# Performance work log

Measured on AMD Instinct MI355X. Metric: run time of the kernel, lower is better.

The kernel has to match this reference:

```python
import jax, jax.numpy as jnp
import numpy as np

B, N, D = 1024, 100, 768  # N=100 is hard-coded by th_embedding Linear(100,1)
EPS_LN, EPS = 1e-5, 1e-8


def setup_inputs() -> dict:
    key = jax.random.key(0)
    k0, k1, k2 = jax.random.split(key, 3)
    return {
        "x": jax.random.normal(k0, (B, N, D), dtype=jnp.float32),
        "cluster_center": jax.random.normal(k1, (B, 1, D), dtype=jnp.float32),
        "alpha": jnp.ones((1,), dtype=jnp.float32),
        "ln_gamma": jnp.ones((D,), dtype=jnp.float32),
        "ln_beta": jnp.zeros((D,), dtype=jnp.float32),
        "th_w": jax.random.normal(k2, (1, N), dtype=jnp.float32) * 0.1,
        "th_b": jnp.zeros((1,), dtype=jnp.float32),
    }


def reference(x, cluster_center, alpha, ln_gamma, ln_beta, th_w, th_b):
    # LayerNorm over last dim
    mu = jnp.mean(x, axis=-1, keepdims=True)
    var = jnp.mean((x - mu) ** 2, axis=-1, keepdims=True)
    xn = (x - mu) / jnp.sqrt(var + EPS_LN) * ln_gamma + ln_beta  # [B,N,D]

    # pairwise cosine similarity  [B,N,N]
    num = jnp.einsum("bnd,bmd->bnm", xn, xn)
    nrm = jnp.linalg.norm(xn, axis=-1, keepdims=True)            # [B,N,1]
    den = nrm * jnp.swapaxes(nrm, -2, -1)                        # [B,N,N]
    cos_sim = num / (den + EPS)

    # density + min-max normalize  [B,N]
    density = jnp.sum(cos_sim, axis=-1)
    d_max = jnp.max(density, axis=-1, keepdims=True)
    d_min = jnp.min(density, axis=-1, keepdims=True)
    density = (density - d_min) / (d_max - d_min + EPS)

    # learned threshold: Flatten -> Linear(100,1) -> Sigmoid, scaled by alpha
    th = jax.nn.sigmoid(density @ th_w.T + th_b) * alpha         # [B,1]

    # ReLU gate + normalize
    density = jax.nn.relu(density - th)
    density_th = density / (jnp.sum(density, axis=1, keepdims=True) + EPS)

    # weighted shift of cluster center
    distance_map = xn - cluster_center                           # [B,N,D] (broadcast of repeat)
    shift = distance_map * density_th[:, :, None]
    shift_avg = jnp.mean(shift, axis=1, keepdims=True)           # [B,1,D]
    return cluster_center + shift_avg
```

## Files before the change

### kernel.cpp

```cpp
#include <hip/hip_runtime.h>
#include <math.h>

#define BT     1024
#define NROW   100
#define DDIM   768
#define EPS_LN 1e-5f
#define EPSF   1e-8f

#define LDS_BYTES 157876

__device__ __forceinline__ float bflo(unsigned int p) {
    union { unsigned int u; float f; } c; c.u = p << 16; return c.f;
}
__device__ __forceinline__ float bfhi(unsigned int p) {
    union { unsigned int u; float f; } c; c.u = p & 0xFFFF0000u; return c.f;
}
__device__ __forceinline__ unsigned int cvtpk(float lo, float hi) {
    unsigned int r;
    asm("v_cvt_pk_bf16_f32 %0, %1, %2" : "=v"(r) : "v"(lo), "v"(hi));
    return r;
}
__device__ __forceinline__ float wave_sum(float v) {
#pragma unroll
    for (int m = 32; m >= 1; m >>= 1) v += __shfl_xor(v, m, 64);
    return v;
}

#define DPPADD(v, ctrl) \
    v += __int_as_float(__builtin_amdgcn_update_dpp(0, __float_as_int(v), ctrl, 0xf, 0xf, true))

__device__ __forceinline__ float dpp_half_sum(float v) {
    DPPADD(v, 0x111);
    DPPADD(v, 0x112);
    DPPADD(v, 0x114);
    DPPADD(v, 0x118);
    DPPADD(v, 0x142);
    return v;
}
__device__ __forceinline__ float dpp_half_sum_bcast(float v) {
    v = dpp_half_sum(v);
    return __int_as_float(__builtin_amdgcn_ds_swizzle(__float_as_int(v), 0x03E0));
}

extern "C" __global__ void __launch_bounds__(BT, 4)
ccs_kernel(const float* __restrict__ x,
           const float* __restrict__ cc,
           const float* __restrict__ alpha,
           const float* __restrict__ gamma,
           const float* __restrict__ beta,
           const float* __restrict__ thw,
           const float* __restrict__ thb,
           float* __restrict__ out)
{
    extern __shared__ char lds[];
    unsigned int* u   = (unsigned int*)lds;
    float* S    = (float*)(lds + 153600);
    float* nrm  = (float*)(lds + 156672);
    float* dens = (float*)(lds + 157072);
    float* w2   = (float*)(lds + 157472);
    float* Wsh  = (float*)(lds + 157872);

    const int tid = threadIdx.x;
    const int w   = tid >> 6;
    const int l   = tid & 63;
    const int li  = l & 31;
    const int hw  = (w << 1) | (l >> 5);
    const int b   = blockIdx.x;
    const float* xb = x + (size_t)b * (NROW * DDIM);

    const int base = 4 * li;
    const int pcnt = (hw < 4) ? 4 : 3;

    float xf[24];
    {
        const float* xr = xb + hw * DDIM + base;
#pragma unroll
        for (int k = 0; k < 6; ++k)
            *(float4*)&xf[4 * k] = *(const float4*)(xr + 128 * k);
    }

    float thwa = 0.f, thwb = 0.f, alphav = 0.f, thbv = 0.f;
    if (w == 0) {
        thwa = thw[l];
        if (l < NROW - 64) thwb = thw[64 + l];
        alphav = alpha[0];
        thbv   = thb[0];
    }
    float2 ccv = make_float2(0.f, 0.f);
    if (tid < 384) ccv = *(const float2*)(cc + (size_t)b * DDIM + 2 * tid);

    uint2 gpk[3], bpk[3];
#pragma unroll
    for (int k = 0; k < 3; ++k) {
        const float4 g4 = *(const float4*)(gamma + 256 * k + base);
        const float4 g5 = *(const float4*)(gamma + 256 * k + 128 + base);
        const float4 b4 = *(const float4*)(beta  + 256 * k + base);
        const float4 b5 = *(const float4*)(beta  + 256 * k + 128 + base);
        gpk[k].x = cvtpk(g4.x, g4.y); gpk[k].y = cvtpk(g4.z, g4.w);
        bpk[k].x = cvtpk(b4.x, b4.y); bpk[k].y = cvtpk(b4.z, b4.w);
        (void)g5; (void)b5;
    }
    uint2 gp6[6], bp6[6];
#pragma unroll
    for (int k = 0; k < 6; ++k) {
        const float4 g4 = *(const float4*)(gamma + 128 * k + base);
        const float4 b4 = *(const float4*)(beta  + 128 * k + base);
        gp6[k].x = cvtpk(g4.x, g4.y); gp6[k].y = cvtpk(g4.z, g4.w);
        bp6[k].x = cvtpk(b4.x, b4.y); bp6[k].y = cvtpk(b4.z, b4.w);
    }

#pragma unroll
    for (int r = 0; r < 4; ++r) {
        if (r >= pcnt) break;
        const int row = hw + 32 * r;

        float p0 = 0.f, p1 = 0.f;
#pragma unroll
        for (int m = 0; m < 24; ++m) { p0 += xf[m]; p1 = fmaf(xf[m], xf[m], p1); }

        float xn1[24];
        if (r + 1 < pcnt) {
            const float* xr = xb + (row + 32) * DDIM + base;
#pragma unroll
            for (int k = 0; k < 6; ++k)
                *(float4*)&xn1[4 * k] = *(const float4*)(xr + 128 * k);
        }

        p0 = dpp_half_sum_bcast(p0);
        p1 = dpp_half_sum_bcast(p1);
        const float mu   = p0 * (1.0f / DDIM);
        const float var  = p1 * (1.0f / DDIM) - mu * mu;
        const float A    = rsqrtf(var + EPS_LN);
        const float nmuA = -mu * A;

        float q = 0.f;
#pragma unroll
        for (int k = 0; k < 6; ++k) {
            const float g0 = bflo(gp6[k].x), g1 = bfhi(gp6[k].x);
            const float g2 = bflo(gp6[k].y), g3 = bfhi(gp6[k].y);
            const float b0 = bflo(bp6[k].x), b1 = bfhi(bp6[k].x);
            const float b2 = bflo(bp6[k].y), b3 = bfhi(bp6[k].y);
            float t, v;
            t = fmaf(xf[4*k+0], A, nmuA); v = fmaf(t, g0, b0); xf[4*k+0] = v; q = fmaf(v, v, q);
            t = fmaf(xf[4*k+1], A, nmuA); v = fmaf(t, g1, b1); xf[4*k+1] = v; q = fmaf(v, v, q);
            t = fmaf(xf[4*k+2], A, nmuA); v = fmaf(t, g2, b2); xf[4*k+2] = v; q = fmaf(v, v, q);
            t = fmaf(xf[4*k+3], A, nmuA); v = fmaf(t, g3, b3); xf[4*k+3] = v; q = fmaf(v, v, q);
        }
        q = dpp_half_sum_bcast(q);
        const float qc  = fmaxf(q, 1e-30f);
        const float inv = rsqrtf(qc);
        const float nr  = qc * inv;

        unsigned int* ur = u + row * 384 + 2 * li;
#pragma unroll
        for (int k = 0; k < 6; ++k) {
            uint2 pk;
            pk.x = cvtpk(xf[4 * k + 0] * inv, xf[4 * k + 1] * inv);
            pk.y = cvtpk(xf[4 * k + 2] * inv, xf[4 * k + 3] * inv);
            *(uint2*)&ur[64 * k] = pk;
        }
        if (li == 0) nrm[row] = nr;

        if (r + 1 < pcnt) {
#pragma unroll
            for (int m = 0; m < 24; ++m) xf[m] = xn1[m];
        }
    }
    __syncthreads();

    if (tid < 384) {
        float ax = 0.f, ay = 0.f;
        const unsigned int* up = u + tid;
#pragma unroll 4
        for (int n = 0; n < NROW; ++n) {
            const unsigned int pw = up[n * 384];
            ax += bflo(pw); ay += bfhi(pw);
        }
        *(float2*)&S[2 * tid] = make_float2(ax, ay);
    }
    __syncthreads();

    {
        float Sv[24];
#pragma unroll
        for (int k = 0; k < 3; ++k) {
            *(float4*)&Sv[8 * k]     = *(const float4*)&S[256 * k + 8 * li];
            *(float4*)&Sv[8 * k + 4] = *(const float4*)&S[256 * k + 8 * li + 4];
        }
#pragma unroll
        for (int r = 0; r < 4; ++r) {
            if (r >= pcnt) break;
            const int row = hw + 32 * r;
            const unsigned int* ur = u + row * 384 + 4 * li;
            float d = 0.f;
#pragma unroll
            for (int k = 0; k < 3; ++k) {
                const uint4 pw = *(const uint4*)&ur[128 * k];
                d = fmaf(bflo(pw.x), Sv[8*k+0], d); d = fmaf(bfhi(pw.x), Sv[8*k+1], d);
                d = fmaf(bflo(pw.y), Sv[8*k+2], d); d = fmaf(bfhi(pw.y), Sv[8*k+3], d);
                d = fmaf(bflo(pw.z), Sv[8*k+4], d); d = fmaf(bfhi(pw.z), Sv[8*k+5], d);
                d = fmaf(bflo(pw.w), Sv[8*k+6], d); d = fmaf(bfhi(pw.w), Sv[8*k+7], d);
            }
            d = dpp_half_sum(d);
            if (li == 31) dens[row] = d;
        }
    }
    __syncthreads();

    if (w == 0) {
        const float va = dens[l];
        const bool  hb = (l < NROW - 64);
        const float vb = hb ? dens[64 + l] : 0.f;

        float mxv = hb ? fmaxf(va, vb) : va;
        float mnv = hb ? fminf(va, vb) : va;
#pragma unroll
        for (int m = 32; m >= 1; m >>= 1) {
            mxv = fmaxf(mxv, __shfl_xor(mxv, m, 64));
            mnv = fminf(mnv, __shfl_xor(mnv, m, 64));
        }
        const float rng = 1.0f / (mxv - mnv + EPSF);
        const float ra  = (va - mnv) * rng;
        const float rb  = (vb - mnv) * rng;

        float td = ra * thwa + (hb ? rb * thwb : 0.f);
        td = wave_sum(td);
        const float z  = td + thbv;
        const float th = alphav / (1.0f + expf(-z));

        const float ga  = fmaxf(ra - th, 0.f);
        const float gb_ = hb ? fmaxf(rb - th, 0.f) : 0.f;
        const float sg  = wave_sum(ga + gb_);
        const float wf  = 1.0f / (sg + EPSF);

        w2[l] = ga * wf * nrm[l];
        if (hb) w2[64 + l] = gb_ * wf * nrm[64 + l];
        if (l == 0) Wsh[0] = sg * wf;
    }
    __syncthreads();

    if (tid < 384) {
        float ax = 0.f, ay = 0.f;
        const unsigned int* up = u + tid;
#pragma unroll 4
        for (int n = 0; n < NROW; ++n) {
            const float wv = w2[n];
            const unsigned int pw = up[n * 384];
            ax = fmaf(wv, bflo(pw), ax); ay = fmaf(wv, bfhi(pw), ay);
        }
        const float W = Wsh[0];
        float2 o;
        o.x = ccv.x + (ax - ccv.x * W) * (1.0f / NROW);
        o.y = ccv.y + (ay - ccv.y * W) * (1.0f / NROW);
        *(float2*)(out + (size_t)b * DDIM + 2 * tid) = o;
    }
}

extern "C" void kernel_launch(void* const* d_in, const int* in_sizes, int n_in,
                              void* d_out, int out_size, void* d_ws, size_t ws_size,
                              hipStream_t stream) {
    const float* x     = (const float*)d_in[0];
    const float* cc    = (const float*)d_in[1];
    const float* alpha = (const float*)d_in[2];
    const float* gamma = (const float*)d_in[3];
    const float* beta  = (const float*)d_in[4];
    const float* thw   = (const float*)d_in[5];
    const float* thb   = (const float*)d_in[6];
    float* out = (float*)d_out;

    ccs_kernel<<<1024, BT, LDS_BYTES, stream>>>(x, cc, alpha, gamma, beta, thw, thb, out);
}
```

Baseline: 81.19 us.

## Make kernel persistent over four batches and prefetch next batch rows during tail phases

Launches 256 persistent blocks that each handle four batch items instead of one block per item. While the current item runs its reduction, density and weighted-sum phases, each block prefetches the first two rows of the next item into registers so global loads overlap compute. It also drops an unused gamma/beta packing loop. The cost is higher register pressure and an extra barrier per item, and with only 256 blocks on a 256-CU device each CU holds a single 1024-thread block, so within-block overlap must replace the latency hiding that block-level concurrency used to give.

New measurement: 172.9 us. 2.13x slower.

```diff
diff --git a/kernel.cpp b/kernel.cpp
--- a/kernel.cpp
+++ b/kernel.cpp
@@ -2,6 +2,8 @@
 #include <math.h>
 
 #define BT     1024
+#define GRID   256
+#define NITEMS 4
 #define NROW   100
 #define DDIM   768
 #define EPS_LN 1e-5f
@@ -66,17 +68,19 @@
     const int li  = l & 31;
     const int hw  = (w << 1) | (l >> 5);
     const int b   = blockIdx.x;
-    const float* xb = x + (size_t)b * (NROW * DDIM);
-
     const int base = 4 * li;
-    const int pcnt = (hw < 4) ? 4 : 3;
-
-    float xf[24];
+    const bool has4 = (hw < 4);
+    const int pcnt = has4 ? 4 : 3;
+
+    float pf0[24], pf1[24];
     {
-        const float* xr = xb + hw * DDIM + base;
-#pragma unroll
-        for (int k = 0; k < 6; ++k)
-            *(float4*)&xf[4 * k] = *(const float4*)(xr + 128 * k);
+        const float* xr0 = x + (size_t)b * (NROW * DDIM) + hw * DDIM + base;
+        const float* xr1 = x + (size_t)b * (NROW * DDIM) + (hw + 32) * DDIM + base;
+#pragma unroll
+        for (int k = 0; k < 6; ++k) {
+            *(float4*)&pf0[4 * k] = *(const float4*)(xr0 + 128 * k);
+            *(float4*)&pf1[4 * k] = *(const float4*)(xr1 + 128 * k);
+        }
     }
 
     float thwa = 0.f, thwb = 0.f, alphav = 0.f, thbv = 0.f;
@@ -86,20 +90,7 @@
         alphav = alpha[0];
         thbv   = thb[0];
     }
-    float2 ccv = make_float2(0.f, 0.f);
-    if (tid < 384) ccv = *(const float2*)(cc + (size_t)b * DDIM + 2 * tid);
-
-    uint2 gpk[3], bpk[3];
-#pragma unroll
-    for (int k = 0; k < 3; ++k) {
-        const float4 g4 = *(const float4*)(gamma + 256 * k + base);
-        const float4 g5 = *(const float4*)(gamma + 256 * k + 128 + base);
-        const float4 b4 = *(const float4*)(beta  + 256 * k + base);
-        const float4 b5 = *(const float4*)(beta  + 256 * k + 128 + base);
-        gpk[k].x = cvtpk(g4.x, g4.y); gpk[k].y = cvtpk(g4.z, g4.w);
-        bpk[k].x = cvtpk(b4.x, b4.y); bpk[k].y = cvtpk(b4.z, b4.w);
-        (void)g5; (void)b5;
-    }
+
     uint2 gp6[6], bp6[6];
 #pragma unroll
     for (int k = 0; k < 6; ++k) {
@@ -109,23 +100,10 @@
         bp6[k].x = cvtpk(b4.x, b4.y); bp6[k].y = cvtpk(b4.z, b4.w);
     }
 
-#pragma unroll
-    for (int r = 0; r < 4; ++r) {
-        if (r >= pcnt) break;
-        const int row = hw + 32 * r;
-
+    auto process_row = [&](float (&xf)[24], int row) {
         float p0 = 0.f, p1 = 0.f;
 #pragma unroll
         for (int m = 0; m < 24; ++m) { p0 += xf[m]; p1 = fmaf(xf[m], xf[m], p1); }
-
-        float xn1[24];
-        if (r + 1 < pcnt) {
-            const float* xr = xb + (row + 32) * DDIM + base;
-#pragma unroll
-            for (int k = 0; k < 6; ++k)
-                *(float4*)&xn1[4 * k] = *(const float4*)(xr + 128 * k);
-        }
-
         p0 = dpp_half_sum_bcast(p0);
         p1 = dpp_half_sum_bcast(p1);
         const float mu   = p0 * (1.0f / DDIM);
@@ -160,99 +138,133 @@
             *(uint2*)&ur[64 * k] = pk;
         }
         if (li == 0) nrm[row] = nr;
-
-        if (r + 1 < pcnt) {
-#pragma unroll
-            for (int m = 0; m < 24; ++m) xf[m] = xn1[m];
-        }
-    }
-    __syncthreads();
-
-    if (tid < 384) {
-        float ax = 0.f, ay = 0.f;
-        const unsigned int* up = u + tid;
+    };
+
+    for (int it = 0; it < NITEMS; ++it) {
+        const int bi = b + GRID * it;
+        const float* xb = x + (size_t)bi * (NROW * DDIM);
+
+        float2 ccv = make_float2(0.f, 0.f);
+        if (tid < 384) ccv = *(const float2*)(cc + (size_t)bi * DDIM + 2 * tid);
+
+        float A24[24];
+        {
+            const float* xr = xb + (hw + 64) * DDIM + base;
+#pragma unroll
+            for (int k = 0; k < 6; ++k)
+                *(float4*)&A24[4 * k] = *(const float4*)(xr + 128 * k);
+        }
+        process_row(pf0, hw);
+
+        float B24[24];
+        if (has4) {
+            const float* xr = xb + (hw + 96) * DDIM + base;
+#pragma unroll
+            for (int k = 0; k < 6; ++k)
+                *(float4*)&B24[4 * k] = *(const float4*)(xr + 128 * k);
+        }
+        process_row(pf1, hw + 32);
+        process_row(A24, hw + 64);
+        if (has4) process_row(B24, hw + 96);
+
+        if (it + 1 < NITEMS) {
+            const float* xr0 = x + (size_t)(bi + GRID) * (NROW * DDIM) + hw * DDIM + base;
+            const float* xr1 = x + (size_t)(bi + GRID) * (NROW * DDIM) + (hw + 32) * DDIM + base;
+#pragma unroll
+            for (int k = 0; k < 6; ++k) {
+                *(float4*)&pf0[4 * k] = *(const float4*)(xr0 + 128 * k);
+                *(float4*)&pf1[4 * k] = *(const float4*)(xr1 + 128 * k);
+            }
+        }
+        __syncthreads();
+
+        if (tid < 384) {
+            float ax = 0.f, ay = 0.f;
+            const unsigned int* up = u + tid;
 #pragma unroll 4
-        for (int n = 0; n < NROW; ++n) {
-            const unsigned int pw = up[n * 384];
-            ax += bflo(pw); ay += bfhi(pw);
-        }
-        *(float2*)&S[2 * tid] = make_float2(ax, ay);
-    }
-    __syncthreads();
-
-    {
-        float Sv[24];
-#pragma unroll
-        for (int k = 0; k < 3; ++k) {
-            *(float4*)&Sv[8 * k]     = *(const float4*)&S[256 * k + 8 * li];
-            *(float4*)&Sv[8 * k + 4] = *(const float4*)&S[256 * k + 8 * li + 4];
-        }
-#pragma unroll
-        for (int r = 0; r < 4; ++r) {
-            if (r >= pcnt) break;
-            const int row = hw + 32 * r;
-            const unsigned int* ur = u + row * 384 + 4 * li;
-            float d = 0.f;
+            for (int n = 0; n < NROW; ++n) {
+                const unsigned int pw = up[n * 384];
+                ax += bflo(pw); ay += bfhi(pw);
+            }
+            *(float2*)&S[2 * tid] = make_float2(ax, ay);
+        }
+        __syncthreads();
+
+        {
+            float Sv[24];
 #pragma unroll
             for (int k = 0; k < 3; ++k) {
-                const uint4 pw = *(const uint4*)&ur[128 * k];
-                d = fmaf(bflo(pw.x), Sv[8*k+0], d); d = fmaf(bfhi(pw.x), Sv[8*k+1], d);
-                d = fmaf(bflo(pw.y), Sv[8*k+2], d); d = fmaf(bfhi(pw.y), Sv[8*k+3], d);
-                d = fmaf(bflo(pw.z), Sv[8*k+4], d); d = fmaf(bfhi(pw.z), Sv[8*k+5], d);
-                d = fmaf(bflo(pw.w), Sv[8*k+6], d); d = fmaf(bfhi(pw.w), Sv[8*k+7], d);
-            }
-            d = dpp_half_sum(d);
-            if (li == 31) dens[row] = d;
-        }
-    }
-    __syncthreads();
-
-    if (w == 0) {
-        const float va = dens[l];
-        const bool  hb = (l < NROW - 64);
-        const float vb = hb ? dens[64 + l] : 0.f;
-
-        float mxv = hb ? fmaxf(va, vb) : va;
-        float mnv = hb ? fminf(va, vb) : va;
-#pragma unroll
-        for (int m = 32; m >= 1; m >>= 1) {
-            mxv = fmaxf(mxv, __shfl_xor(mxv, m, 64));
-            mnv = fminf(mnv, __shfl_xor(mnv, m, 64));
-        }
-        const float rng = 1.0f / (mxv - mnv + EPSF);
-        const float ra  = (va - mnv) * rng;
-        const float rb  = (vb - mnv) * rng;
-
-        float td = ra * thwa + (hb ? rb * thwb : 0.f);
-        td = wave_sum(td);
-        const float z  = td + thbv;
-        const float th = alphav / (1.0f + expf(-z));
-
-        const float ga  = fmaxf(ra - th, 0.f);
-        const float gb_ = hb ? fmaxf(rb - th, 0.f) : 0.f;
-        const float sg  = wave_sum(ga + gb_);
-        const float wf  = 1.0f / (sg + EPSF);
-
-        w2[l] = ga * wf * nrm[l];
-        if (hb) w2[64 + l] = gb_ * wf * nrm[64 + l];
-        if (l == 0) Wsh[0] = sg * wf;
-    }
-    __syncthreads();
-
-    if (tid < 384) {
-        float ax = 0.f, ay = 0.f;
-        const unsigned int* up = u + tid;
+                *(float4*)&Sv[8 * k]     = *(const float4*)&S[256 * k + 8 * li];
+                *(float4*)&Sv[8 * k + 4] = *(const float4*)&S[256 * k + 8 * li + 4];
+            }
+#pragma unroll
+            for (int r = 0; r < 4; ++r) {
+                if (r >= pcnt) break;
+                const int row = hw + 32 * r;
+                const unsigned int* ur = u + row * 384 + 4 * li;
+                float d = 0.f;
+#pragma unroll
+                for (int k = 0; k < 3; ++k) {
+                    const uint4 pw = *(const uint4*)&ur[128 * k];
+                    d = fmaf(bflo(pw.x), Sv[8*k+0], d); d = fmaf(bfhi(pw.x), Sv[8*k+1], d);
+                    d = fmaf(bflo(pw.y), Sv[8*k+2], d); d = fmaf(bfhi(pw.y), Sv[8*k+3], d);
+                    d = fmaf(bflo(pw.z), Sv[8*k+4], d); d = fmaf(bfhi(pw.z), Sv[8*k+5], d);
+                    d = fmaf(bflo(pw.w), Sv[8*k+6], d); d = fmaf(bfhi(pw.w), Sv[8*k+7], d);
+                }
+                d = dpp_half_sum(d);
+                if (li == 31) dens[row] = d;
+            }
+        }
+        __syncthreads();
+
+        if (w == 0) {
+            const float va = dens[l];
+            const bool  hb = (l < NROW - 64);
+            const float vb = hb ? dens[64 + l] : 0.f;
+
+            float mxv = hb ? fmaxf(va, vb) : va;
+            float mnv = hb ? fminf(va, vb) : va;
+#pragma unroll
+            for (int m = 32; m >= 1; m >>= 1) {
+                mxv = fmaxf(mxv, __shfl_xor(mxv, m, 64));
+                mnv = fminf(mnv, __shfl_xor(mnv, m, 64));
+            }
+            const float rng = 1.0f / (mxv - mnv + EPSF);
+            const float ra  = (va - mnv) * rng;
+            const float rb  = (vb - mnv) * rng;
+
+            float td = ra * thwa + (hb ? rb * thwb : 0.f);
+            td = wave_sum(td);
+            const float z  = td + thbv;
+            const float th = alphav / (1.0f + expf(-z));
+
+            const float ga  = fmaxf(ra - th, 0.f);
+            const float gb_ = hb ? fmaxf(rb - th, 0.f) : 0.f;
+            const float sg  = wave_sum(ga + gb_);
+            const float wf  = 1.0f / (sg + EPSF);
+
+            w2[l] = ga * wf * nrm[l];
+            if (hb) w2[64 + l] = gb_ * wf * nrm[64 + l];
+            if (l == 0) Wsh[0] = sg * wf;
+        }
+        __syncthreads();
+
+        if (tid < 384) {
+            float ax = 0.f, ay = 0.f;
+            const unsigned int* up = u + tid;
 #pragma unroll 4
-        for (int n = 0; n < NROW; ++n) {
-            const float wv = w2[n];
-            const unsigned int pw = up[n * 384];
-            ax = fmaf(wv, bflo(pw), ax); ay = fmaf(wv, bfhi(pw), ay);
-        }
-        const float W = Wsh[0];
-        float2 o;
-        o.x = ccv.x + (ax - ccv.x * W) * (1.0f / NROW);
-        o.y = ccv.y + (ay - ccv.y * W) * (1.0f / NROW);
-        *(float2*)(out + (size_t)b * DDIM + 2 * tid) = o;
+            for (int n = 0; n < NROW; ++n) {
+                const float wv = w2[n];
+                const unsigned int pw = up[n * 384];
+                ax = fmaf(wv, bflo(pw), ax); ay = fmaf(wv, bfhi(pw), ay);
+            }
+            const float W = Wsh[0];
+            float2 o;
+            o.x = ccv.x + (ax - ccv.x * W) * (1.0f / NROW);
+            o.y = ccv.y + (ay - ccv.y * W) * (1.0f / NROW);
+            *(float2*)(out + (size_t)bi * DDIM + 2 * tid) = o;
+        }
+        __syncthreads();
     }
 }
 
@@ -268,5 +280,5 @@
     const float* thb   = (const float*)d_in[6];
     float* out = (float*)d_out;
 
-    ccs_kernel<<<1024, BT, LDS_BYTES, stream>>>(x, cc, alpha, gamma, beta, thw, thb, out);
-}
+    ccs_kernel<<<GRID, BT, LDS_BYTES, stream>>>(x, cc, alpha, gamma, beta, thw, thb, out);
+}
```

## Make kernel persistent over 4 batches with cross-item prefetch of next x rows

Applied to the files above, without the earlier changes.

The grid shrinks from 1024 blocks to 256 persistent blocks, each looping over 4 batch items. The next item's first x rows are prefetched during the last row of the current item, which hides global load latency across items and avoids relaunching blocks. __syncthreads is replaced by a custom lgkmcnt wait plus s_barrier, and dead gamma/beta packing is removed. The risk is serialization inside each block: with only 256 blocks at one block per CU, the cross-block overlap the 1024-block grid used to provide to hide latency is lost.

Result: slower. 100.0 us (+23.2%).

```diff
diff --git a/kernel.cpp b/kernel.cpp
--- a/kernel.cpp
+++ b/kernel.cpp
@@ -2,12 +2,16 @@
 #include <math.h>
 
 #define BT     1024
+#define GRID   256
+#define NITEMS 4
 #define NROW   100
 #define DDIM   768
 #define EPS_LN 1e-5f
 #define EPSF   1e-8f
 
 #define LDS_BYTES 157876
+
+#define TBAR() asm volatile("s_waitcnt lgkmcnt(0)\n\ts_barrier" ::: "memory")
 
 __device__ __forceinline__ float bflo(unsigned int p) {
     union { unsigned int u; float f; } c; c.u = p << 16; return c.f;
@@ -66,14 +70,12 @@
     const int li  = l & 31;
     const int hw  = (w << 1) | (l >> 5);
     const int b   = blockIdx.x;
-    const float* xb = x + (size_t)b * (NROW * DDIM);
-
     const int base = 4 * li;
     const int pcnt = (hw < 4) ? 4 : 3;
 
     float xf[24];
     {
-        const float* xr = xb + hw * DDIM + base;
+        const float* xr = x + (size_t)b * (NROW * DDIM) + hw * DDIM + base;
 #pragma unroll
         for (int k = 0; k < 6; ++k)
             *(float4*)&xf[4 * k] = *(const float4*)(xr + 128 * k);
@@ -86,20 +88,7 @@
         alphav = alpha[0];
         thbv   = thb[0];
     }
-    float2 ccv = make_float2(0.f, 0.f);
-    if (tid < 384) ccv = *(const float2*)(cc + (size_t)b * DDIM + 2 * tid);
-
-    uint2 gpk[3], bpk[3];
-#pragma unroll
-    for (int k = 0; k < 3; ++k) {
-        const float4 g4 = *(const float4*)(gamma + 256 * k + base);
-        const float4 g5 = *(const float4*)(gamma + 256 * k + 128 + base);
-        const float4 b4 = *(const float4*)(beta  + 256 * k + base);
-        const float4 b5 = *(const float4*)(beta  + 256 * k + 128 + base);
-        gpk[k].x = cvtpk(g4.x, g4.y); gpk[k].y = cvtpk(g4.z, g4.w);
-        bpk[k].x = cvtpk(b4.x, b4.y); bpk[k].y = cvtpk(b4.z, b4.w);
-        (void)g5; (void)b5;
-    }
+
     uint2 gp6[6], bp6[6];
 #pragma unroll
     for (int k = 0; k < 6; ++k) {
@@ -109,150 +98,166 @@
         bp6[k].x = cvtpk(b4.x, b4.y); bp6[k].y = cvtpk(b4.z, b4.w);
     }
 
-#pragma unroll
-    for (int r = 0; r < 4; ++r) {
-        if (r >= pcnt) break;
-        const int row = hw + 32 * r;
-
-        float p0 = 0.f, p1 = 0.f;
-#pragma unroll
-        for (int m = 0; m < 24; ++m) { p0 += xf[m]; p1 = fmaf(xf[m], xf[m], p1); }
-
-        float xn1[24];
-        if (r + 1 < pcnt) {
-            const float* xr = xb + (row + 32) * DDIM + base;
-#pragma unroll
-            for (int k = 0; k < 6; ++k)
-                *(float4*)&xn1[4 * k] = *(const float4*)(xr + 128 * k);
-        }
-
-        p0 = dpp_half_sum_bcast(p0);
-        p1 = dpp_half_sum_bcast(p1);
-        const float mu   = p0 * (1.0f / DDIM);
-        const float var  = p1 * (1.0f / DDIM) - mu * mu;
-        const float A    = rsqrtf(var + EPS_LN);
-        const float nmuA = -mu * A;
-
-        float q = 0.f;
-#pragma unroll
-        for (int k = 0; k < 6; ++k) {
-            const float g0 = bflo(gp6[k].x), g1 = bfhi(gp6[k].x);
-            const float g2 = bflo(gp6[k].y), g3 = bfhi(gp6[k].y);
-            const float b0 = bflo(bp6[k].x), b1 = bfhi(bp6[k].x);
-            const float b2 = bflo(bp6[k].y), b3 = bfhi(bp6[k].y);
-            float t, v;
-            t = fmaf(xf[4*k+0], A, nmuA); v = fmaf(t, g0, b0); xf[4*k+0] = v; q = fmaf(v, v, q);
-            t = fmaf(xf[4*k+1], A, nmuA); v = fmaf(t, g1, b1); xf[4*k+1] = v; q = fmaf(v, v, q);
-            t = fmaf(xf[4*k+2], A, nmuA); v = fmaf(t, g2, b2); xf[4*k+2] = v; q = fmaf(v, v, q);
-            t = fmaf(xf[4*k+3], A, nmuA); v = fmaf(t, g3, b3); xf[4*k+3] = v; q = fmaf(v, v, q);
-        }
-        q = dpp_half_sum_bcast(q);
-        const float qc  = fmaxf(q, 1e-30f);
-        const float inv = rsqrtf(qc);
-        const float nr  = qc * inv;
-
-        unsigned int* ur = u + row * 384 + 2 * li;
-#pragma unroll
-        for (int k = 0; k < 6; ++k) {
-            uint2 pk;
-            pk.x = cvtpk(xf[4 * k + 0] * inv, xf[4 * k + 1] * inv);
-            pk.y = cvtpk(xf[4 * k + 2] * inv, xf[4 * k + 3] * inv);
-            *(uint2*)&ur[64 * k] = pk;
-        }
-        if (li == 0) nrm[row] = nr;
-
-        if (r + 1 < pcnt) {
-#pragma unroll
-            for (int m = 0; m < 24; ++m) xf[m] = xn1[m];
-        }
-    }
-    __syncthreads();
-
-    if (tid < 384) {
-        float ax = 0.f, ay = 0.f;
-        const unsigned int* up = u + tid;
-#pragma unroll 4
-        for (int n = 0; n < NROW; ++n) {
-            const unsigned int pw = up[n * 384];
-            ax += bflo(pw); ay += bfhi(pw);
-        }
-        *(float2*)&S[2 * tid] = make_float2(ax, ay);
-    }
-    __syncthreads();
-
-    {
-        float Sv[24];
-#pragma unroll
-        for (int k = 0; k < 3; ++k) {
-            *(float4*)&Sv[8 * k]     = *(const float4*)&S[256 * k + 8 * li];
-            *(float4*)&Sv[8 * k + 4] = *(const float4*)&S[256 * k + 8 * li + 4];
-        }
+    for (int it = 0; it < NITEMS; ++it) {
+        const int bi = b + GRID * it;
+        const float* xb = x + (size_t)bi * (NROW * DDIM);
+
+        float2 ccv = make_float2(0.f, 0.f);
+        if (tid < 384) ccv = *(const float2*)(cc + (size_t)bi * DDIM + 2 * tid);
+
 #pragma unroll
         for (int r = 0; r < 4; ++r) {
             if (r >= pcnt) break;
             const int row = hw + 32 * r;
-            const unsigned int* ur = u + row * 384 + 4 * li;
-            float d = 0.f;
+
+            float p0 = 0.f, p1 = 0.f;
+#pragma unroll
+            for (int m = 0; m < 24; ++m) { p0 += xf[m]; p1 = fmaf(xf[m], xf[m], p1); }
+
+            const bool nx    = (r + 1 < pcnt);
+            const bool nitem = (!nx) && (it + 1 < NITEMS);
+            float xn1[24];
+            if (nx) {
+                const float* xr = xb + (row + 32) * DDIM + base;
+#pragma unroll
+                for (int k = 0; k < 6; ++k)
+                    *(float4*)&xn1[4 * k] = *(const float4*)(xr + 128 * k);
+            } else if (nitem) {
+                const float* xr = x + (size_t)(bi + GRID) * (NROW * DDIM) + hw * DDIM + base;
+#pragma unroll
+                for (int k = 0; k < 6; ++k)
+                    *(float4*)&xn1[4 * k] = *(const float4*)(xr + 128 * k);
+            }
+
+            p0 = dpp_half_sum_bcast(p0);
+            p1 = dpp_half_sum_bcast(p1);
+            const float mu   = p0 * (1.0f / DDIM);
+            const float var  = p1 * (1.0f / DDIM) - mu * mu;
+            const float A    = rsqrtf(var + EPS_LN);
+            const float nmuA = -mu * A;
+
+            float q = 0.f;
+#pragma unroll
+            for (int k = 0; k < 6; ++k) {
+                const float g0 = bflo(gp6[k].x), g1 = bfhi(gp6[k].x);
+                const float g2 = bflo(gp6[k].y), g3 = bfhi(gp6[k].y);
+                const float b0 = bflo(bp6[k].x), b1 = bfhi(bp6[k].x);
+                const float b2 = bflo(bp6[k].y), b3 = bfhi(bp6[k].y);
+                float t, v;
+                t = fmaf(xf[4*k+0], A, nmuA); v = fmaf(t, g0, b0); xf[4*k+0] = v; q = fmaf(v, v, q);
+                t = fmaf(xf[4*k+1], A, nmuA); v = fmaf(t, g1, b1); xf[4*k+1] = v; q = fmaf(v, v, q);
+                t = fmaf(xf[4*k+2], A, nmuA); v = fmaf(t, g2, b2); xf[4*k+2] = v; q = fmaf(v, v, q);
+                t = fmaf(xf[4*k+3], A, nmuA); v = fmaf(t, g3, b3); xf[4*k+3] = v; q = fmaf(v, v, q);
+            }
+            q = dpp_half_sum_bcast(q);
+            const float qc  = fmaxf(q, 1e-30f);
+            const float inv = rsqrtf(qc);
+            const float nr  = qc * inv;
+
+            unsigned int* ur = u + row * 384 + 2 * li;
+#pragma unroll
+            for (int k = 0; k < 6; ++k) {
+                uint2 pk;
+                pk.x = cvtpk(xf[4 * k + 0] * inv, xf[4 * k + 1] * inv);
+                pk.y = cvtpk(xf[4 * k + 2] * inv, xf[4 * k + 3] * inv);
+                *(uint2*)&ur[64 * k] = pk;
+            }
+            if (li == 0) nrm[row] = nr;
+
+            if (nx || nitem) {
+#pragma unroll
+                for (int m = 0; m < 24; ++m) xf[m] = xn1[m];
+            }
+        }
+        TBAR();
+
+        if (tid < 384) {
+            float ax = 0.f, ay = 0.f;
+            const unsigned int* up = u + tid;
+#pragma unroll 4
+            for (int n = 0; n < NROW; ++n) {
+                const unsigned int pw = up[n * 384];
+                ax += bflo(pw); ay += bfhi(pw);
+            }
+            *(float2*)&S[2 * tid] = make_float2(ax, ay);
+        }
+        TBAR();
+
+        {
+            float Sv[24];
 #pragma unroll
             for (int k = 0; k < 3; ++k) {
-                const uint4 pw = *(const uint4*)&ur[128 * k];
-                d = fmaf(bflo(pw.x), Sv[8*k+0], d); d = fmaf(bfhi(pw.x), Sv[8*k+1], d);
-                d = fmaf(bflo(pw.y), Sv[8*k+2], d); d = fmaf(bfhi(pw.y), Sv[8*k+3], d);
-                d = fmaf(bflo(pw.z), Sv[8*k+4], d); d = fmaf(bfhi(pw.z), Sv[8*k+5], d);
-                d = fmaf(bflo(pw.w), Sv[8*k+6], d); d = fmaf(bfhi(pw.w), Sv[8*k+7], d);
-            }
-            d = dpp_half_sum(d);
-            if (li == 31) dens[row] = d;
-        }
-    }
-    __syncthreads();
-
-    if (w == 0) {
-        const float va = dens[l];
-        const bool  hb = (l < NROW - 64);
-        const float vb = hb ? dens[64 + l] : 0.f;
-
-        float mxv = hb ? fmaxf(va, vb) : va;
-        float mnv = hb ? fminf(va, vb) : va;
-#pragma unroll
-        for (int m = 32; m >= 1; m >>= 1) {
-            mxv = fmaxf(mxv, __shfl_xor(mxv, m, 64));
-            mnv = fminf(mnv, __shfl_xor(mnv, m, 64));
-        }
-        const float rng = 1.0f / (mxv - mnv + EPSF);
-        const float ra  = (va - mnv) * rng;
-        const float rb  = (vb - mnv) * rng;
-
-        float td = ra * thwa + (hb ? rb * thwb : 0.f);
-        td = wave_sum(td);
-        const float z  = td + thbv;
-        const float th = alphav / (1.0f + expf(-z));
-
-        const float ga  = fmaxf(ra - th, 0.f);
-        const float gb_ = hb ? fmaxf(rb - th, 0.f) : 0.f;
-        const float sg  = wave_sum(ga + gb_);
-        const float wf  = 1.0f / (sg + EPSF);
-
-        w2[l] = ga * wf * nrm[l];
-        if (hb) w2[64 + l] = gb_ * wf * nrm[64 + l];
-        if (l == 0) Wsh[0] = sg * wf;
-    }
-    __syncthreads();
-
-    if (tid < 384) {
-        float ax = 0.f, ay = 0.f;
-        const unsigned int* up = u + tid;
+                *(float4*)&Sv[8 * k]     = *(const float4*)&S[256 * k + 8 * li];
+                *(float4*)&Sv[8 * k + 4] = *(const float4*)&S[256 * k + 8 * li + 4];
+            }
+#pragma unroll
+            for (int r = 0; r < 4; ++r) {
+                if (r >= pcnt) break;
+                const int row = hw + 32 * r;
+                const unsigned int* ur = u + row * 384 + 4 * li;
+                float d = 0.f;
+#pragma unroll
+                for (int k = 0; k < 3; ++k) {
+                    const uint4 pw = *(const uint4*)&ur[128 * k];
+                    d = fmaf(bflo(pw.x), Sv[8*k+0], d); d = fmaf(bfhi(pw.x), Sv[8*k+1], d);
+                    d = fmaf(bflo(pw.y), Sv[8*k+2], d); d = fmaf(bfhi(pw.y), Sv[8*k+3], d);
+                    d = fmaf(bflo(pw.z), Sv[8*k+4], d); d = fmaf(bfhi(pw.z), Sv[8*k+5], d);
+                    d = fmaf(bflo(pw.w), Sv[8*k+6], d); d = fmaf(bfhi(pw.w), Sv[8*k+7], d);
+                }
+                d = dpp_half_sum(d);
+                if (li == 31) dens[row] = d;
+            }
+        }
+        TBAR();
+
+        if (w == 0) {
+            const float va = dens[l];
+            const bool  hb = (l < NROW - 64);
+            const float vb = hb ? dens[64 + l] : 0.f;
+
+            float mxv = hb ? fmaxf(va, vb) : va;
+            float mnv = hb ? fminf(va, vb) : va;
+#pragma unroll
+            for (int m = 32; m >= 1; m >>= 1) {
+                mxv = fmaxf(mxv, __shfl_xor(mxv, m, 64));
+                mnv = fminf(mnv, __shfl_xor(mnv, m, 64));
+            }
+            const float rng = 1.0f / (mxv - mnv + EPSF);
+            const float ra  = (va - mnv) * rng;
+            const float rb  = (vb - mnv) * rng;
+
+            float td = ra * thwa + (hb ? rb * thwb : 0.f);
+            td = wave_sum(td);
+            const float z  = td + thbv;
+            const float th = alphav / (1.0f + expf(-z));
+
+            const float ga  = fmaxf(ra - th, 0.f);
+            const float gb_ = hb ? fmaxf(rb - th, 0.f) : 0.f;
+            const float sg  = wave_sum(ga + gb_);
+            const float wf  = 1.0f / (sg + EPSF);
+
+            w2[l] = ga * wf * nrm[l];
+            if (hb) w2[64 + l] = gb_ * wf * nrm[64 + l];
+            if (l == 0) Wsh[0] = sg * wf;
+        }
+        TBAR();
+
+        if (tid < 384) {
+            float ax = 0.f, ay = 0.f;
+            const unsigned int* up = u + tid;
 #pragma unroll 4
-        for (int n = 0; n < NROW; ++n) {
-            const float wv = w2[n];
-            const unsigned int pw = up[n * 384];
-            ax = fmaf(wv, bflo(pw), ax); ay = fmaf(wv, bfhi(pw), ay);
-        }
-        const float W = Wsh[0];
-        float2 o;
-        o.x = ccv.x + (ax - ccv.x * W) * (1.0f / NROW);
-        o.y = ccv.y + (ay - ccv.y * W) * (1.0f / NROW);
-        *(float2*)(out + (size_t)b * DDIM + 2 * tid) = o;
+            for (int n = 0; n < NROW; ++n) {
+                const float wv = w2[n];
+                const unsigned int pw = up[n * 384];
+                ax = fmaf(wv, bflo(pw), ax); ay = fmaf(wv, bfhi(pw), ay);
+            }
+            const float W = Wsh[0];
+            float2 o;
+            o.x = ccv.x + (ax - ccv.x * W) * (1.0f / NROW);
+            o.y = ccv.y + (ay - ccv.y * W) * (1.0f / NROW);
+            *(float2*)(out + (size_t)bi * DDIM + 2 * tid) = o;
+        }
+        TBAR();
     }
 }
 
@@ -268,5 +273,5 @@
     const float* thb   = (const float*)d_in[6];
     float* out = (float*)d_out;
 
-    ccs_kernel<<<1024, BT, LDS_BYTES, stream>>>(x, cc, alpha, gamma, beta, thw, thb, out);
-}
+    ccs_kernel<<<GRID, BT, LDS_BYTES, stream>>>(x, cc, alpha, gamma, beta, thw, thb, out);
+}
```

## Process two batch items per block and rebalance LayerNorm rows across half-waves

Applied to the files above, without the earlier changes.

The grid is halved so each block loops over two batch items, spreading gamma/beta setup over more work. Rows 96-99 are now normalised by four waves, each row split across two half-waves, before the main three-row loop, so every half-wave does an equal three rows instead of some doing four. The aim is to shorten the critical path of the normalisation phase and cut per-block overhead. In exchange, only one block fits per CU (large LDS), so fewer blocks in flight may reduce latency hiding. A sync between items is added because the LDS buffers are reused.

Measured after the change: 104.3 us. 28.5% more time.

```diff
diff --git a/kernel.cpp b/kernel.cpp
--- a/kernel.cpp
+++ b/kernel.cpp
@@ -2,6 +2,8 @@
 #include <math.h>
 
 #define BT     1024
+#define GRID   512
+#define NITEMS 2
 #define NROW   100
 #define DDIM   768
 #define EPS_LN 1e-5f
@@ -64,20 +66,11 @@
     const int w   = tid >> 6;
     const int l   = tid & 63;
     const int li  = l & 31;
-    const int hw  = (w << 1) | (l >> 5);
+    const int hi  = l >> 5;
+    const int hw  = (w << 1) | hi;
     const int b   = blockIdx.x;
-    const float* xb = x + (size_t)b * (NROW * DDIM);
-
     const int base = 4 * li;
-    const int pcnt = (hw < 4) ? 4 : 3;
-
-    float xf[24];
-    {
-        const float* xr = xb + hw * DDIM + base;
-#pragma unroll
-        for (int k = 0; k < 6; ++k)
-            *(float4*)&xf[4 * k] = *(const float4*)(xr + 128 * k);
-    }
+    const int pc2 = (hw < 4) ? 4 : 3;
 
     float thwa = 0.f, thwb = 0.f, alphav = 0.f, thbv = 0.f;
     if (w == 0) {
@@ -86,20 +79,7 @@
         alphav = alpha[0];
         thbv   = thb[0];
     }
-    float2 ccv = make_float2(0.f, 0.f);
-    if (tid < 384) ccv = *(const float2*)(cc + (size_t)b * DDIM + 2 * tid);
-
-    uint2 gpk[3], bpk[3];
-#pragma unroll
-    for (int k = 0; k < 3; ++k) {
-        const float4 g4 = *(const float4*)(gamma + 256 * k + base);
-        const float4 g5 = *(const float4*)(gamma + 256 * k + 128 + base);
-        const float4 b4 = *(const float4*)(beta  + 256 * k + base);
-        const float4 b5 = *(const float4*)(beta  + 256 * k + 128 + base);
-        gpk[k].x = cvtpk(g4.x, g4.y); gpk[k].y = cvtpk(g4.z, g4.w);
-        bpk[k].x = cvtpk(b4.x, b4.y); bpk[k].y = cvtpk(b4.z, b4.w);
-        (void)g5; (void)b5;
-    }
+
     uint2 gp6[6], bp6[6];
 #pragma unroll
     for (int k = 0; k < 6; ++k) {
@@ -109,150 +89,217 @@
         bp6[k].x = cvtpk(b4.x, b4.y); bp6[k].y = cvtpk(b4.z, b4.w);
     }
 
-#pragma unroll
-    for (int r = 0; r < 4; ++r) {
-        if (r >= pcnt) break;
-        const int row = hw + 32 * r;
-
-        float p0 = 0.f, p1 = 0.f;
-#pragma unroll
-        for (int m = 0; m < 24; ++m) { p0 += xf[m]; p1 = fmaf(xf[m], xf[m], p1); }
-
-        float xn1[24];
-        if (r + 1 < pcnt) {
-            const float* xr = xb + (row + 32) * DDIM + base;
+    for (int it = 0; it < NITEMS; ++it) {
+        const int bi = b + GRID * it;
+        const float* xb = x + (size_t)bi * (NROW * DDIM);
+
+        float2 ccv = make_float2(0.f, 0.f);
+        if (tid < 384) ccv = *(const float2*)(cc + (size_t)bi * DDIM + 2 * tid);
+
+        if (w < 4) {
+            const int row = 96 + w;
+            float xg[12];
+            {
+                const float* xr = xb + row * DDIM + 384 * hi + base;
+#pragma unroll
+                for (int k = 0; k < 3; ++k)
+                    *(float4*)&xg[4 * k] = *(const float4*)(xr + 128 * k);
+            }
+            float p0 = 0.f, p1 = 0.f;
+#pragma unroll
+            for (int m = 0; m < 12; ++m) { p0 += xg[m]; p1 = fmaf(xg[m], xg[m], p1); }
+            p0 = dpp_half_sum_bcast(p0); p0 += __shfl_xor(p0, 32, 64);
+            p1 = dpp_half_sum_bcast(p1); p1 += __shfl_xor(p1, 32, 64);
+            const float mu   = p0 * (1.0f / DDIM);
+            const float var  = p1 * (1.0f / DDIM) - mu * mu;
+            const float A    = rsqrtf(var + EPS_LN);
+            const float nmuA = -mu * A;
+
+            float q = 0.f;
+#define FW_NORM(KO) \
+            { \
+                _Pragma("unroll") \
+                for (int k = 0; k < 3; ++k) { \
+                    const float g0 = bflo(gp6[KO + k].x), g1 = bfhi(gp6[KO + k].x); \
+                    const float g2 = bflo(gp6[KO + k].y), g3 = bfhi(gp6[KO + k].y); \
+                    const float b0 = bflo(bp6[KO + k].x), b1 = bfhi(bp6[KO + k].x); \
+                    const float b2 = bflo(bp6[KO + k].y), b3 = bfhi(bp6[KO + k].y); \
+                    float t, v; \
+                    t = fmaf(xg[4*k+0], A, nmuA); v = fmaf(t, g0, b0); xg[4*k+0] = v; q = fmaf(v, v, q); \
+                    t = fmaf(xg[4*k+1], A, nmuA); v = fmaf(t, g1, b1); xg[4*k+1] = v; q = fmaf(v, v, q); \
+                    t = fmaf(xg[4*k+2], A, nmuA); v = fmaf(t, g2, b2); xg[4*k+2] = v; q = fmaf(v, v, q); \
+                    t = fmaf(xg[4*k+3], A, nmuA); v = fmaf(t, g3, b3); xg[4*k+3] = v; q = fmaf(v, v, q); \
+                } \
+            }
+            if (hi == 0) { FW_NORM(0) } else { FW_NORM(3) }
+            q = dpp_half_sum_bcast(q); q += __shfl_xor(q, 32, 64);
+            const float qc  = fmaxf(q, 1e-30f);
+            const float inv = rsqrtf(qc);
+            const float nr  = qc * inv;
+
+            unsigned int* ur = u + row * 384 + 192 * hi + 2 * li;
+#pragma unroll
+            for (int k = 0; k < 3; ++k) {
+                uint2 pk;
+                pk.x = cvtpk(xg[4 * k + 0] * inv, xg[4 * k + 1] * inv);
+                pk.y = cvtpk(xg[4 * k + 2] * inv, xg[4 * k + 3] * inv);
+                *(uint2*)&ur[64 * k] = pk;
+            }
+            if (l == 0) nrm[row] = nr;
+        }
+
+        float xf[24];
+        {
+            const float* xr = xb + hw * DDIM + base;
 #pragma unroll
             for (int k = 0; k < 6; ++k)
-                *(float4*)&xn1[4 * k] = *(const float4*)(xr + 128 * k);
-        }
-
-        p0 = dpp_half_sum_bcast(p0);
-        p1 = dpp_half_sum_bcast(p1);
-        const float mu   = p0 * (1.0f / DDIM);
-        const float var  = p1 * (1.0f / DDIM) - mu * mu;
-        const float A    = rsqrtf(var + EPS_LN);
-        const float nmuA = -mu * A;
-
-        float q = 0.f;
-#pragma unroll
-        for (int k = 0; k < 6; ++k) {
-            const float g0 = bflo(gp6[k].x), g1 = bfhi(gp6[k].x);
-            const float g2 = bflo(gp6[k].y), g3 = bfhi(gp6[k].y);
-            const float b0 = bflo(bp6[k].x), b1 = bfhi(bp6[k].x);
-            const float b2 = bflo(bp6[k].y), b3 = bfhi(bp6[k].y);
-            float t, v;
-            t = fmaf(xf[4*k+0], A, nmuA); v = fmaf(t, g0, b0); xf[4*k+0] = v; q = fmaf(v, v, q);
-            t = fmaf(xf[4*k+1], A, nmuA); v = fmaf(t, g1, b1); xf[4*k+1] = v; q = fmaf(v, v, q);
-            t = fmaf(xf[4*k+2], A, nmuA); v = fmaf(t, g2, b2); xf[4*k+2] = v; q = fmaf(v, v, q);
-            t = fmaf(xf[4*k+3], A, nmuA); v = fmaf(t, g3, b3); xf[4*k+3] = v; q = fmaf(v, v, q);
-        }
-        q = dpp_half_sum_bcast(q);
-        const float qc  = fmaxf(q, 1e-30f);
-        const float inv = rsqrtf(qc);
-        const float nr  = qc * inv;
-
-        unsigned int* ur = u + row * 384 + 2 * li;
-#pragma unroll
-        for (int k = 0; k < 6; ++k) {
-            uint2 pk;
-            pk.x = cvtpk(xf[4 * k + 0] * inv, xf[4 * k + 1] * inv);
-            pk.y = cvtpk(xf[4 * k + 2] * inv, xf[4 * k + 3] * inv);
-            *(uint2*)&ur[64 * k] = pk;
-        }
-        if (li == 0) nrm[row] = nr;
-
-        if (r + 1 < pcnt) {
-#pragma unroll
-            for (int m = 0; m < 24; ++m) xf[m] = xn1[m];
-        }
-    }
-    __syncthreads();
-
-    if (tid < 384) {
-        float ax = 0.f, ay = 0.f;
-        const unsigned int* up = u + tid;
+                *(float4*)&xf[4 * k] = *(const float4*)(xr + 128 * k);
+        }
+#pragma unroll
+        for (int r = 0; r < 3; ++r) {
+            const int row = hw + 32 * r;
+
+            float p0 = 0.f, p1 = 0.f;
+#pragma unroll
+            for (int m = 0; m < 24; ++m) { p0 += xf[m]; p1 = fmaf(xf[m], xf[m], p1); }
+
+            float xn1[24];
+            if (r < 2) {
+                const float* xr = xb + (row + 32) * DDIM + base;
+#pragma unroll
+                for (int k = 0; k < 6; ++k)
+                    *(float4*)&xn1[4 * k] = *(const float4*)(xr + 128 * k);
+            }
+
+            p0 = dpp_half_sum_bcast(p0);
+            p1 = dpp_half_sum_bcast(p1);
+            const float mu   = p0 * (1.0f / DDIM);
+            const float var  = p1 * (1.0f / DDIM) - mu * mu;
+            const float A    = rsqrtf(var + EPS_LN);
+            const float nmuA = -mu * A;
+
+            float q = 0.f;
+#pragma unroll
+            for (int k = 0; k < 6; ++k) {
+                const float g0 = bflo(gp6[k].x), g1 = bfhi(gp6[k].x);
+                const float g2 = bflo(gp6[k].y), g3 = bfhi(gp6[k].y);
+                const float b0 = bflo(bp6[k].x), b1 = bfhi(bp6[k].x);
+                const float b2 = bflo(bp6[k].y), b3 = bfhi(bp6[k].y);
+                float t, v;
+                t = fmaf(xf[4*k+0], A, nmuA); v = fmaf(t, g0, b0); xf[4*k+0] = v; q = fmaf(v, v, q);
+                t = fmaf(xf[4*k+1], A, nmuA); v = fmaf(t, g1, b1); xf[4*k+1] = v; q = fmaf(v, v, q);
+                t = fmaf(xf[4*k+2], A, nmuA); v = fmaf(t, g2, b2); xf[4*k+2] = v; q = fmaf(v, v, q);
+                t = fmaf(xf[4*k+3], A, nmuA); v = fmaf(t, g3, b3); xf[4*k+3] = v; q = fmaf(v, v, q);
+            }
+            q = dpp_half_sum_bcast(q);
+            const float qc  = fmaxf(q, 1e-30f);
+            const float inv = rsqrtf(qc);
+            const float nr  = qc * inv;
+
+            unsigned int* ur = u + row * 384 + 2 * li;
+#pragma unroll
+            for (int k = 0; k < 6; ++k) {
+                uint2 pk;
+                pk.x = cvtpk(xf[4 * k + 0] * inv, xf[4 * k + 1] * inv);
+                pk.y = cvtpk(xf[4 * k + 2] * inv, xf[4 * k + 3] * inv);
+                *(uint2*)&ur[64 * k] = pk;
+            }
+            if (li == 0) nrm[row] = nr;
+
+            if (r < 2) {
+#pragma unroll
+                for (int m = 0; m < 24; ++m) xf[m] = xn1[m];
+            }
+        }
+        __syncthreads();
+
+        if (tid < 384) {
+            float ax = 0.f, ay = 0.f;
+            const unsigned int* up = u + tid;
 #pragma unroll 4
-        for (int n = 0; n < NROW; ++n) {
-            const unsigned int pw = up[n * 384];
-            ax += bflo(pw); ay += bfhi(pw);
-        }
-        *(float2*)&S[2 * tid] = make_float2(ax, ay);
-    }
-    __syncthreads();
-
-    {
-        float Sv[24];
-#pragma unroll
-        for (int k = 0; k < 3; ++k) {
-            *(float4*)&Sv[8 * k]     = *(const float4*)&S[256 * k + 8 * li];
-            *(float4*)&Sv[8 * k + 4] = *(const float4*)&S[256 * k + 8 * li + 4];
-        }
-#pragma unroll
-        for (int r = 0; r < 4; ++r) {
-            if (r >= pcnt) break;
-            const int row = hw + 32 * r;
-            const unsigned int* ur = u + row * 384 + 4 * li;
-            float d = 0.f;
+            for (int n = 0; n < NROW; ++n) {
+                const unsigned int pw = up[n * 384];
+                ax += bflo(pw); ay += bfhi(pw);
+            }
+            *(float2*)&S[2 * tid] = make_float2(ax, ay);
+        }
+        __syncthreads();
+
+        {
+            float Sv[24];
 #pragma unroll
             for (int k = 0; k < 3; ++k) {
-                const uint4 pw = *(const uint4*)&ur[128 * k];
-                d = fmaf(bflo(pw.x), Sv[8*k+0], d); d = fmaf(bfhi(pw.x), Sv[8*k+1], d);
-                d = fmaf(bflo(pw.y), Sv[8*k+2], d); d = fmaf(bfhi(pw.y), Sv[8*k+3], d);
-                d = fmaf(bflo(pw.z), Sv[8*k+4], d); d = fmaf(bfhi(pw.z), Sv[8*k+5], d);
-                d = fmaf(bflo(pw.w), Sv[8*k+6], d); d = fmaf(bfhi(pw.w), Sv[8*k+7], d);
-            }
-            d = dpp_half_sum(d);
-            if (li == 31) dens[row] = d;
-        }
-    }
-    __syncthreads();
-
-    if (w == 0) {
-        const float va = dens[l];
-        const bool  hb = (l < NROW - 64);
-        const float vb = hb ? dens[64 + l] : 0.f;
-
-        float mxv = hb ? fmaxf(va, vb) : va;
-        float mnv = hb ? fminf(va, vb) : va;
-#pragma unroll
-        for (int m = 32; m >= 1; m >>= 1) {
-            mxv = fmaxf(mxv, __shfl_xor(mxv, m, 64));
-            mnv = fminf(mnv, __shfl_xor(mnv, m, 64));
-        }
-        const float rng = 1.0f / (mxv - mnv + EPSF);
-        const float ra  = (va - mnv) * rng;
-        const float rb  = (vb - mnv) * rng;
-
-        float td = ra * thwa + (hb ? rb * thwb : 0.f);
-        td = wave_sum(td);
-        const float z  = td + thbv;
-        const float th = alphav / (1.0f + expf(-z));
-
-        const float ga  = fmaxf(ra - th, 0.f);
-        const float gb_ = hb ? fmaxf(rb - th, 0.f) : 0.f;
-        const float sg  = wave_sum(ga + gb_);
-        const float wf  = 1.0f / (sg + EPSF);
-
-        w2[l] = ga * wf * nrm[l];
-        if (hb) w2[64 + l] = gb_ * wf * nrm[64 + l];
-        if (l == 0) Wsh[0] = sg * wf;
-    }
-    __syncthreads();
-
-    if (tid < 384) {
-        float ax = 0.f, ay = 0.f;
-        const unsigned int* up = u + tid;
+                *(float4*)&Sv[8 * k]     = *(const float4*)&S[256 * k + 8 * li];
+                *(float4*)&Sv[8 * k + 4] = *(const float4*)&S[256 * k + 8 * li + 4];
+            }
+#pragma unroll
+            for (int r = 0; r < 4; ++r) {
+                if (r >= pc2) break;
+                const int row = hw + 32 * r;
+                const unsigned int* ur = u + row * 384 + 4 * li;
+                float d = 0.f;
+#pragma unroll
+                for (int k = 0; k < 3; ++k) {
+                    const uint4 pw = *(const uint4*)&ur[128 * k];
+                    d = fmaf(bflo(pw.x), Sv[8*k+0], d); d = fmaf(bfhi(pw.x), Sv[8*k+1], d);
+                    d = fmaf(bflo(pw.y), Sv[8*k+2], d); d = fmaf(bfhi(pw.y), Sv[8*k+3], d);
+                    d = fmaf(bflo(pw.z), Sv[8*k+4], d); d = fmaf(bfhi(pw.z), Sv[8*k+5], d);
+                    d = fmaf(bflo(pw.w), Sv[8*k+6], d); d = fmaf(bfhi(pw.w), Sv[8*k+7], d);
+                }
+                d = dpp_half_sum(d);
+                if (li == 31) dens[row] = d;
+            }
+        }
+        __syncthreads();
+
+        if (w == 0) {
+            const float va = dens[l];
+            const bool  hb = (l < NROW - 64);
+            const float vb = hb ? dens[64 + l] : 0.f;
+
+            float mxv = hb ? fmaxf(va, vb) : va;
+            float mnv = hb ? fminf(va, vb) : va;
+#pragma unroll
+            for (int m = 32; m >= 1; m >>= 1) {
+                mxv = fmaxf(mxv, __shfl_xor(mxv, m, 64));
+                mnv = fminf(mnv, __shfl_xor(mnv, m, 64));
+            }
+            const float rng = 1.0f / (mxv - mnv + EPSF);
+            const float ra  = (va - mnv) * rng;
+            const float rb  = (vb - mnv) * rng;
+
+            float td = ra * thwa + (hb ? rb * thwb : 0.f);
+            td = wave_sum(td);
+            const float z  = td + thbv;
+            const float th = alphav / (1.0f + expf(-z));
+
+            const float ga  = fmaxf(ra - th, 0.f);
+            const float gb_ = hb ? fmaxf(rb - th, 0.f) : 0.f;
+            const float sg  = wave_sum(ga + gb_);
+            const float wf  = 1.0f / (sg + EPSF);
+
+            w2[l] = ga * wf * nrm[l];
+            if (hb) w2[64 + l] = gb_ * wf * nrm[64 + l];
+            if (l == 0) Wsh[0] = sg * wf;
+        }
+        __syncthreads();
+
+        if (tid < 384) {
+            float ax = 0.f, ay = 0.f;
+            const unsigned int* up = u + tid;
 #pragma unroll 4
-        for (int n = 0; n < NROW; ++n) {
-            const float wv = w2[n];
-            const unsigned int pw = up[n * 384];
-            ax = fmaf(wv, bflo(pw), ax); ay = fmaf(wv, bfhi(pw), ay);
-        }
-        const float W = Wsh[0];
-        float2 o;
-        o.x = ccv.x + (ax - ccv.x * W) * (1.0f / NROW);
-        o.y = ccv.y + (ay - ccv.y * W) * (1.0f / NROW);
-        *(float2*)(out + (size_t)b * DDIM + 2 * tid) = o;
+            for (int n = 0; n < NROW; ++n) {
+                const float wv = w2[n];
+                const unsigned int pw = up[n * 384];
+                ax = fmaf(wv, bflo(pw), ax); ay = fmaf(wv, bfhi(pw), ay);
+            }
+            const float W = Wsh[0];
+            float2 o;
+            o.x = ccv.x + (ax - ccv.x * W) * (1.0f / NROW);
+            o.y = ccv.y + (ay - ccv.y * W) * (1.0f / NROW);
+            *(float2*)(out + (size_t)bi * DDIM + 2 * tid) = o;
+        }
+        if (it + 1 < NITEMS) __syncthreads();
     }
 }
 
@@ -268,5 +315,5 @@
     const float* thb   = (const float*)d_in[6];
     float* out = (float*)d_out;
 
-    ccs_kernel<<<1024, BT, LDS_BYTES, stream>>>(x, cc, alpha, gamma, beta, thw, thb, out);
-}
+    ccs_kernel<<<GRID, BT, LDS_BYTES, stream>>>(x, cc, alpha, gamma, beta, thw, thb, out);
+}
```
